# Optimization experiments

Hardware: AMD Instinct MI355X
Metric: run time of the kernel (lower is better)

Reference implementation:

```python
import jax, jax.numpy as jnp
import numpy as np

N = 50000   # nodes
E = 800000  # edges (avg degree 16)
D = 256     # node feature dim
H = 4       # heads per layer
C = 64      # per-head channels
L = 3       # depth
SCALE = 1.0 / (C ** 0.5)


def setup_inputs() -> dict:
    key = jax.random.key(0)
    ks = jax.random.split(key, 11)
    w = 0.05
    return {
        "x": jax.random.normal(ks[0], (N, D), jnp.float32),
        "edge_index": jax.random.randint(ks[1], (2, E), 0, N, dtype=jnp.int32),
        "Wq": jax.random.normal(ks[2], (L, D, H * C), jnp.float32) * w,
        "bq": jax.random.normal(ks[3], (L, H * C), jnp.float32) * w,
        "Wk": jax.random.normal(ks[4], (L, D, H * C), jnp.float32) * w,
        "bk": jax.random.normal(ks[5], (L, H * C), jnp.float32) * w,
        "Wv": jax.random.normal(ks[6], (L, D, H * C), jnp.float32) * w,
        "bv": jax.random.normal(ks[7], (L, H * C), jnp.float32) * w,
        "Ws": jax.random.normal(ks[8], (L, D, H * C), jnp.float32) * w,
        "bs": jax.random.normal(ks[9], (L, H * C), jnp.float32) * w,
    }


def _segment_softmax(alpha, seg, num_segments):
    # alpha: [E, H], seg: [E] destination node ids
    amax = jax.ops.segment_max(alpha, seg, num_segments=num_segments)  # [N, H]
    amax = jnp.where(jnp.isfinite(amax), amax, 0.0)  # isolated nodes -> -inf
    ex = jnp.exp(alpha - amax[seg])
    denom = jax.ops.segment_sum(ex, seg, num_segments=num_segments)  # [N, H]
    return ex / (denom[seg] + 1e-16)


def reference(x, edge_index, Wq, bq, Wk, bk, Wv, bv, Ws, bs):
    # PyG TransformerConv, heads=H, concat=True, root_weight=True, no edge features.
    src = edge_index[0]  # message source j
    dst = edge_index[1]  # message target i
    h = x
    for l in range(L):
        q = (h @ Wq[l] + bq[l]).reshape(N, H, C)
        k = (h @ Wk[l] + bk[l]).reshape(N, H, C)
        v = (h @ Wv[l] + bv[l]).reshape(N, H, C)
        # per-edge attention logits [E, H]
        alpha = jnp.einsum('ehc,ehc->eh', q[dst], k[src]) * SCALE
        attn = _segment_softmax(alpha, dst, N)
        # weighted message aggregation: [E, H, C] -> [N, H, C]
        msg = v[src] * attn[..., None]
        agg = jax.ops.segment_sum(msg, dst, num_segments=N).reshape(N, H * C)
        h = jax.nn.relu(agg + h @ Ws[l] + bs[l])
    return h
```

## Files before the change

### kernel.cpp

```cpp
#include <hip/hip_runtime.h>
#include <hip/hip_bf16.h>
#include <math.h>

#define N_NODES 50000
#define N_EDGES 800000
#define ATT_SCALE 0.125f

typedef __attribute__((ext_vector_type(8))) short bf16x8;
typedef __attribute__((ext_vector_type(4))) float f32x4;

__device__ __forceinline__ unsigned short f2bf(float f) {
  __hip_bfloat16 h = __float2bfloat16(f);
  unsigned short u; __builtin_memcpy(&u, &h, 2); return u;
}
__device__ __forceinline__ float bf2f(unsigned short u) {
  __hip_bfloat16 h; __builtin_memcpy(&h, &u, 2); return __bfloat162float(h);
}
__device__ __forceinline__ void gload16(const void* g, void* l) {
  __builtin_amdgcn_global_load_lds(
      (const __attribute__((address_space(1))) unsigned int*)g,
      (__attribute__((address_space(3))) unsigned int*)l, 16, 0, 0);
}

__global__ void zero_int(int* __restrict__ p, int n) {
  int i = blockIdx.x * blockDim.x + threadIdx.x;
  if (i < n) p[i] = 0;
}

__global__ void hist_kernel(const int* __restrict__ dst, int* __restrict__ counts, int e) {
  int i = blockIdx.x * blockDim.x + threadIdx.x;
  if (i < e) atomicAdd(&counts[dst[i]], 1);
}

__global__ __launch_bounds__(1024) void scan1_kernel(const int* __restrict__ counts,
                                                     int* __restrict__ offsets,
                                                     int* __restrict__ btot, int n) {
  __shared__ int wsum[16];
  const int tid = threadIdx.x;
  const int lane = tid & 63, wid = tid >> 6;
  int idx = blockIdx.x * 1024 + tid;
  int v = (idx < n) ? counts[idx] : 0;
  int s = v;
#pragma unroll
  for (int off = 1; off < 64; off <<= 1) {
    int t = __shfl_up(s, off);
    if (lane >= off) s += t;
  }
  if (lane == 63) wsum[wid] = s;
  __syncthreads();
  if (wid == 0) {
    int wsv = (lane < 16) ? wsum[lane] : 0;
#pragma unroll
    for (int off = 1; off < 16; off <<= 1) {
      int t = __shfl_up(wsv, off);
      if (lane >= off) wsv += t;
    }
    if (lane < 16) wsum[lane] = wsv;
  }
  __syncthreads();
  int wbase = (wid > 0) ? wsum[wid - 1] : 0;
  if (idx < n) offsets[idx] = wbase + s - v;
  if (tid == 0) btot[blockIdx.x] = wsum[15];
}

__global__ __launch_bounds__(64) void scan2_kernel(int* __restrict__ btot, int nb) {
  int lane = threadIdx.x;
  int v = (lane < nb) ? btot[lane] : 0;
  int s = v;
#pragma unroll
  for (int off = 1; off < 64; off <<= 1) {
    int t = __shfl_up(s, off);
    if (lane >= off) s += t;
  }
  if (lane < nb) btot[lane] = s - v;
}

__global__ void scan3_kernel(int* __restrict__ offsets, int* __restrict__ cursor,
                             const int* __restrict__ btot, int n) {
  int i = blockIdx.x * blockDim.x + threadIdx.x;
  if (i < n) {
    int o = offsets[i] + btot[i >> 10];
    offsets[i] = o;
    cursor[i] = o;
  }
}

__global__ __launch_bounds__(1024) void scan_kernel(const int* __restrict__ counts,
                                                    int* __restrict__ offsets,
                                                    int* __restrict__ cursor, int n) {
  __shared__ int wsum[16];
  const int tid = threadIdx.x;
  const int lane = tid & 63, wid = tid >> 6;
  int carry = 0;
  for (int base = 0; base < n; base += 1024) {
    int idx = base + tid;
    int v = (idx < n) ? counts[idx] : 0;
    int s = v;
#pragma unroll
    for (int off = 1; off < 64; off <<= 1) {
      int t = __shfl_up(s, off);
      if (lane >= off) s += t;
    }
    if (lane == 63) wsum[wid] = s;
    __syncthreads();
    if (wid == 0) {
      int wsv = (lane < 16) ? wsum[lane] : 0;
#pragma unroll
      for (int off = 1; off < 16; off <<= 1) {
        int t = __shfl_up(wsv, off);
        if (lane >= off) wsv += t;
      }
      if (lane < 16) wsum[lane] = wsv;
    }
    __syncthreads();
    int wbase = (wid > 0) ? wsum[wid - 1] : 0;
    if (idx < n) {
      int ex = carry + wbase + s - v;
      offsets[idx] = ex;
      cursor[idx] = ex;
    }
    int total = wsum[15];
    __syncthreads();
    carry += total;
  }
  if (tid == 0) offsets[n] = carry;
}

__global__ void fill_kernel(const int* __restrict__ src, const int* __restrict__ dst,
                            int* __restrict__ cursor, int* __restrict__ ssrc, int e) {
  int i = blockIdx.x * blockDim.x + threadIdx.x;
  if (i < e) {
    int d = dst[i];
    int slot = atomicAdd(&cursor[d], 1);
    ssrc[slot] = src[i];
  }
}

__global__ void convert_x_kernel(const float* __restrict__ x,
                                 unsigned short* __restrict__ Ahi,
                                 unsigned short* __restrict__ Alo) {
  int t = blockIdx.x * blockDim.x + threadIdx.x;
  int row = t >> 6, g = (t & 63) * 4;
  if (row >= N_NODES) return;
  float4 xv = *(const float4*)(x + (size_t)row * 256 + g);
  ushort4 hi, lo;
  hi.x = f2bf(xv.x); lo.x = f2bf(xv.x - bf2f(hi.x));
  hi.y = f2bf(xv.y); lo.y = f2bf(xv.y - bf2f(hi.y));
  hi.z = f2bf(xv.z); lo.z = f2bf(xv.z - bf2f(hi.z));
  hi.w = f2bf(xv.w); lo.w = f2bf(xv.w - bf2f(hi.w));
  *(ushort4*)(Ahi + (size_t)row * 256 + g) = hi;
  *(ushort4*)(Alo + (size_t)row * 256 + g) = lo;
}

__global__ void convert_w_kernel(const float* __restrict__ Wq, const float* __restrict__ Wk,
                                 const float* __restrict__ Wv, const float* __restrict__ Ws,
                                 unsigned short* __restrict__ Bexp) {
  int t = blockIdx.x * blockDim.x + threadIdx.x;
  if (t >= 3 * 256 * 1024) return;
  int n = t & 1023;
  int k = (t >> 10) & 255;
  int l = t >> 18;
  const float* W = (n < 256) ? Wq : (n < 512) ? Wk : (n < 768) ? Wv : Ws;
  float w = W[l * 65536 + k * 256 + (n & 255)];
  unsigned short hi = f2bf(w);
  unsigned short lo = f2bf(w - bf2f(hi));
  unsigned short* row = Bexp + ((size_t)l * 1024 + n) * 768;
  row[k] = hi; row[256 + k] = lo; row[512 + k] = hi;
}

__global__ __launch_bounds__(256) void bgemm_kernel(
    const unsigned short* __restrict__ Ahi,
    const unsigned short* __restrict__ Alo,
    const unsigned short* __restrict__ B,
    const float* __restrict__ bq, const float* __restrict__ bk,
    const float* __restrict__ bv, const float* __restrict__ bs,
    int layer,
    unsigned short* __restrict__ Qb,
    unsigned short* __restrict__ Kb,
    unsigned short* __restrict__ Vb,
    float* __restrict__ Sf) {
  __shared__ __align__(16) char lds[49152];
  char* Al  = lds;
  char* Bl1 = lds + 16384;
  char* Bl2 = lds + 32768;

  const int orig = blockIdx.x;
  const int swz = (orig & 7) * 391 + (orig >> 3);
  const int nb = swz & 7;
  const int m0 = (swz >> 3) * 128;

  const int tid = threadIdx.x;
  const int wid = tid >> 6;
  const int lane = tid & 63;
  const int l15 = lane & 15, lhi = lane >> 4;
  const int wr = wid >> 1, wc = wid & 1;

  const char* Ag_hi = (const char*)Ahi;
  const char* Ag_lo = (const char*)Alo;
  const char* Bg = (const char*)(B + ((size_t)layer * 1024 + nb * 128) * 768);

  f32x4 acc[4][4];
#pragma unroll
  for (int m = 0; m < 4; m++)
#pragma unroll
    for (int n = 0; n < 4; n++) acc[m][n] = (f32x4){0.f, 0.f, 0.f, 0.f};

  const int swzl = (l15 & 7) << 4;

  for (int kt4 = 0; kt4 < 4; kt4++) {
    const int ka2 = kt4 * 128;
#pragma unroll
    for (int i = 0; i < 4; i++) {
      int o = tid * 16 + i * 4096;
      int row = o >> 7;
      int sg = ((o >> 4) & 7) ^ (row & 7);
      gload16(Ag_hi + (size_t)(m0 + row) * 512 + ka2 + sg * 16, Al  + wid * 1024 + i * 4096);
      gload16(Bg + (size_t)row * 1536 + ka2 + sg * 16,          Bl1 + wid * 1024 + i * 4096);
      gload16(Bg + (size_t)row * 1536 + 512 + ka2 + sg * 16,    Bl2 + wid * 1024 + i * 4096);
    }
    __syncthreads();

    bf16x8 af[2][4], bfrag[2][4];
#pragma unroll
    for (int kk = 0; kk < 2; kk++)
#pragma unroll
      for (int m = 0; m < 4; m++) {
        af[kk][m]    = *(const bf16x8*)(Al  + (wr * 64 + m * 16 + l15) * 128 + ((kk * 64 + lhi * 16) ^ swzl));
        bfrag[kk][m] = *(const bf16x8*)(Bl1 + (wc * 64 + m * 16 + l15) * 128 + ((kk * 64 + lhi * 16) ^ swzl));
      }
#pragma unroll
    for (int kk = 0; kk < 2; kk++)
#pragma unroll
      for (int m = 0; m < 4; m++)
#pragma unroll
        for (int n = 0; n < 4; n++)
          acc[m][n] = __builtin_amdgcn_mfma_f32_16x16x32_bf16(af[kk][m], bfrag[kk][n], acc[m][n], 0, 0, 0);
#pragma unroll
    for (int kk = 0; kk < 2; kk++)
#pragma unroll
      for (int m = 0; m < 4; m++)
        bfrag[kk][m] = *(const bf16x8*)(Bl2 + (wc * 64 + m * 16 + l15) * 128 + ((kk * 64 + lhi * 16) ^ swzl));
#pragma unroll
    for (int kk = 0; kk < 2; kk++)
#pragma unroll
      for (int m = 0; m < 4; m++)
#pragma unroll
        for (int n = 0; n < 4; n++)
          acc[m][n] = __builtin_amdgcn_mfma_f32_16x16x32_bf16(af[kk][m], bfrag[kk][n], acc[m][n], 0, 0, 0);
    __syncthreads();
  }

  for (int kt4 = 0; kt4 < 4; kt4++) {
    const int ka2 = kt4 * 128;
#pragma unroll
    for (int i = 0; i < 4; i++) {
      int o = tid * 16 + i * 4096;
      int row = o >> 7;
      int sg = ((o >> 4) & 7) ^ (row & 7);
      gload16(Ag_lo + (size_t)(m0 + row) * 512 + ka2 + sg * 16, Al  + wid * 1024 + i * 4096);
      gload16(Bg + (size_t)row * 1536 + 1024 + ka2 + sg * 16,   Bl1 + wid * 1024 + i * 4096);
    }
    __syncthreads();

    bf16x8 af[2][4], bfrag[2][4];
#pragma unroll
    for (int kk = 0; kk < 2; kk++)
#pragma unroll
      for (int m = 0; m < 4; m++) {
        af[kk][m]    = *(const bf16x8*)(Al  + (wr * 64 + m * 16 + l15) * 128 + ((kk * 64 + lhi * 16) ^ swzl));
        bfrag[kk][m] = *(const bf16x8*)(Bl1 + (wc * 64 + m * 16 + l15) * 128 + ((kk * 64 + lhi * 16) ^ swzl));
      }
#pragma unroll
    for (int kk = 0; kk < 2; kk++)
#pragma unroll
      for (int m = 0; m < 4; m++)
#pragma unroll
        for (int n = 0; n < 4; n++)
          acc[m][n] = __builtin_amdgcn_mfma_f32_16x16x32_bf16(af[kk][m], bfrag[kk][n], acc[m][n], 0, 0, 0);
    __syncthreads();
  }

  const float* bias = ((nb < 2) ? bq : (nb < 4) ? bk : (nb < 6) ? bv : bs) + layer * 256 + (nb & 1) * 128;
  float bn[4];
#pragma unroll
  for (int n = 0; n < 4; n++) bn[n] = bias[wc * 64 + n * 16 + l15];

  const int col = (nb & 1) * 128 + wc * 64 + l15;
  if (nb < 6) {
    unsigned short* T = (nb < 2) ? Qb : (nb < 4) ? Kb : Vb;
#pragma unroll
    for (int m = 0; m < 4; m++) {
#pragma unroll
      for (int r = 0; r < 4; r++) {
        int row = m0 + wr * 64 + m * 16 + lhi * 4 + r;
        if (row < N_NODES) {
          unsigned short* orow = T + (size_t)row * 256 + col;
#pragma unroll
          for (int n = 0; n < 4; n++) orow[n * 16] = f2bf(acc[m][n][r] + bn[n]);
        }
      }
    }
  } else {
#pragma unroll
    for (int m = 0; m < 4; m++) {
#pragma unroll
      for (int r = 0; r < 4; r++) {
        int row = m0 + wr * 64 + m * 16 + lhi * 4 + r;
        if (row < N_NODES) {
          float* orow = Sf + (size_t)row * 256 + col;
#pragma unroll
          for (int n = 0; n < 4; n++) orow[n * 16] = acc[m][n][r] + bn[n];
        }
      }
    }
  }
}

template <int MODE>
__global__ __launch_bounds__(256) void attn_kernel(
    const unsigned short* __restrict__ Qb,
    const unsigned short* __restrict__ Kb,
    const unsigned short* __restrict__ Vb,
    const float* __restrict__ Sf,
    const int* __restrict__ offsets,
    const int* __restrict__ counts,
    const int* __restrict__ ssrc,
    float* __restrict__ hout,
    unsigned short* __restrict__ Ahi,
    unsigned short* __restrict__ Alo) {
  int wv = threadIdx.x >> 6;
  int lane = threadIdx.x & 63;
  int i = blockIdx.x * 4 + wv;
  if (i >= N_NODES) return;

  const int off = (lane >> 4) * 64 + (lane & 15) * 4;

  ushort4 qb = *(const ushort4*)(Qb + (size_t)i * 256 + off);
  float4 q = make_float4(bf2f(qb.x), bf2f(qb.y), bf2f(qb.z), bf2f(qb.w));

  float mC[4] = {-1e30f, -1e30f, -1e30f, -1e30f};
  float sC[4] = {0.f, 0.f, 0.f, 0.f};
  float4 aC[4];
#pragma unroll
  for (int u = 0; u < 4; u++) aC[u] = make_float4(0.f, 0.f, 0.f, 0.f);

  const int beg = offsets[i];
  const int cnt = counts[i];
  int e = 0;
  for (; e + 4 <= cnt; e += 4) {
    int j[4];
#pragma unroll
    for (int u = 0; u < 4; u++) j[u] = ssrc[beg + e + u];
    ushort4 kk[4], vv[4];
#pragma unroll
    for (int u = 0; u < 4; u++) {
      kk[u] = *(const ushort4*)(Kb + (size_t)j[u] * 256 + off);
      vv[u] = *(const ushort4*)(Vb + (size_t)j[u] * 256 + off);
    }
    float p[4];
#pragma unroll
    for (int u = 0; u < 4; u++)
      p[u] = q.x * bf2f(kk[u].x) + q.y * bf2f(kk[u].y) +
             q.z * bf2f(kk[u].z) + q.w * bf2f(kk[u].w);
#pragma unroll
    for (int u = 0; u < 4; u++) p[u] += __shfl_xor(p[u], 1);
#pragma unroll
    for (int u = 0; u < 4; u++) p[u] += __shfl_xor(p[u], 2);
#pragma unroll
    for (int u = 0; u < 4; u++) p[u] += __shfl_xor(p[u], 4);
#pragma unroll
    for (int u = 0; u < 4; u++) p[u] += __shfl_xor(p[u], 8);
#pragma unroll
    for (int u = 0; u < 4; u++) {
      float pv = p[u] * ATT_SCALE;
      float mn = fmaxf(mC[u], pv);
      float c = __expf(mC[u] - mn);
      float w = __expf(pv - mn);
      sC[u] = sC[u] * c + w;
      aC[u].x = aC[u].x * c + w * bf2f(vv[u].x);
      aC[u].y = aC[u].y * c + w * bf2f(vv[u].y);
      aC[u].z = aC[u].z * c + w * bf2f(vv[u].z);
      aC[u].w = aC[u].w * c + w * bf2f(vv[u].w);
      mC[u] = mn;
    }
  }
  for (; e < cnt; e++) {
    int j1 = ssrc[beg + e];
    ushort4 k1 = *(const ushort4*)(Kb + (size_t)j1 * 256 + off);
    ushort4 v1 = *(const ushort4*)(Vb + (size_t)j1 * 256 + off);
    float p1 = q.x * bf2f(k1.x) + q.y * bf2f(k1.y) + q.z * bf2f(k1.z) + q.w * bf2f(k1.w);
    p1 += __shfl_xor(p1, 1);
    p1 += __shfl_xor(p1, 2);
    p1 += __shfl_xor(p1, 4);
    p1 += __shfl_xor(p1, 8);
    p1 *= ATT_SCALE;
    float mn = fmaxf(mC[0], p1); float c = __expf(mC[0] - mn); float w = __expf(p1 - mn);
    sC[0] = sC[0] * c + w;
    aC[0].x = aC[0].x * c + w * bf2f(v1.x);
    aC[0].y = aC[0].y * c + w * bf2f(v1.y);
    aC[0].z = aC[0].z * c + w * bf2f(v1.z);
    aC[0].w = aC[0].w * c + w * bf2f(v1.w);
    mC[0] = mn;
  }

  float mm = fmaxf(fmaxf(mC[0], mC[1]), fmaxf(mC[2], mC[3]));
  float s = 0.f;
  float4 a = make_float4(0.f, 0.f, 0.f, 0.f);
#pragma unroll
  for (int u = 0; u < 4; u++) {
    float c = __expf(mC[u] - mm);
    s += sC[u] * c;
    a.x += aC[u].x * c;
    a.y += aC[u].y * c;
    a.z += aC[u].z * c;
    a.w += aC[u].w * c;
  }

  float4 sk = *(const float4*)(Sf + (size_t)i * 256 + off);
  float inv = 1.f / (s + 1e-16f);
  float4 o = make_float4(fmaxf(a.x * inv + sk.x, 0.f),
                         fmaxf(a.y * inv + sk.y, 0.f),
                         fmaxf(a.z * inv + sk.z, 0.f),
                         fmaxf(a.w * inv + sk.w, 0.f));
  if (MODE == 0) {
    *(float4*)(hout + (size_t)i * 256 + off) = o;
  } else {
    ushort4 hi, lo;
    hi.x = f2bf(o.x); lo.x = f2bf(o.x - bf2f(hi.x));
    hi.y = f2bf(o.y); lo.y = f2bf(o.y - bf2f(hi.y));
    hi.z = f2bf(o.z); lo.z = f2bf(o.z - bf2f(hi.z));
    hi.w = f2bf(o.w); lo.w = f2bf(o.w - bf2f(hi.w));
    *(ushort4*)(Ahi + (size_t)i * 256 + off) = hi;
    *(ushort4*)(Alo + (size_t)i * 256 + off) = lo;
  }
}

#define BM 128
#define BN 128
#define BK 16
__global__ __launch_bounds__(256) void gemm_kernel(
    const float* __restrict__ X,
    const float* __restrict__ Wq, const float* __restrict__ Wk,
    const float* __restrict__ Wv, const float* __restrict__ Ws,
    const float* __restrict__ bq, const float* __restrict__ bk,
    const float* __restrict__ bv, const float* __restrict__ bs,
    int layer, float* __restrict__ out) {
  __shared__ __align__(16) float As[BK][BM + 4];
  __shared__ __align__(16) float Bs[BK][BN + 4];
  const int m0 = blockIdx.x * BM;
  const int n0 = blockIdx.y * BN;
  const int wsel = n0 >> 8;
  const float* W;
  const float* bias;
  if (wsel == 0)      { W = Wq; bias = bq; }
  else if (wsel == 1) { W = Wk; bias = bk; }
  else if (wsel == 2) { W = Wv; bias = bv; }
  else                { W = Ws; bias = bs; }
  W += (size_t)layer * 256 * 256;
  bias += (size_t)layer * 256;
  const int nc0 = n0 & 255;
  const int tid = threadIdx.x;
  const int tx = tid & 15;
  const int ty = tid >> 4;
  float acc[8][8];
#pragma unroll
  for (int i = 0; i < 8; i++)
#pragma unroll
    for (int j = 0; j < 8; j++) acc[i][j] = 0.f;
  for (int k0 = 0; k0 < 256; k0 += BK) {
#pragma unroll
    for (int i = 0; i < 8; i++) {
      int idx = tid + i * 256;
      int r = idx >> 4, c = idx & 15;
      int gr = m0 + r;
      As[c][r] = (gr < N_NODES) ? X[(size_t)gr * 256 + k0 + c] : 0.f;
    }
#pragma unroll
    for (int i = 0; i < 8; i++) {
      int idx = tid + i * 256;
      int r = idx >> 7, c = idx & 127;
      Bs[r][c] = W[(size_t)(k0 + r) * 256 + nc0 + c];
    }
    __syncthreads();
#pragma unroll
    for (int k = 0; k < BK; k++) {
      float4 a0 = *(const float4*)&As[k][ty * 8];
      float4 a1 = *(const float4*)&As[k][ty * 8 + 4];
      float4 b0 = *(const float4*)&Bs[k][tx * 8];
      float4 b1 = *(const float4*)&Bs[k][tx * 8 + 4];
      float a[8] = {a0.x, a0.y, a0.z, a0.w, a1.x, a1.y, a1.z, a1.w};
      float b[8] = {b0.x, b0.y, b0.z, b0.w, b1.x, b1.y, b1.z, b1.w};
#pragma unroll
      for (int mi = 0; mi < 8; mi++)
#pragma unroll
        for (int ni = 0; ni < 8; ni++) acc[mi][ni] = fmaf(a[mi], b[ni], acc[mi][ni]);
    }
    __syncthreads();
  }
  float bl[8];
#pragma unroll
  for (int ni = 0; ni < 8; ni++) bl[ni] = bias[nc0 + tx * 8 + ni];
#pragma unroll
  for (int mi = 0; mi < 8; mi++) {
    int row = m0 + ty * 8 + mi;
    if (row < N_NODES) {
      float* orow = out + (size_t)row * 1024 + n0 + tx * 8;
      float4 o0 = make_float4(acc[mi][0] + bl[0], acc[mi][1] + bl[1],
                              acc[mi][2] + bl[2], acc[mi][3] + bl[3]);
      float4 o1 = make_float4(acc[mi][4] + bl[4], acc[mi][5] + bl[5],
                              acc[mi][6] + bl[6], acc[mi][7] + bl[7]);
      *(float4*)orow = o0;
      *(float4*)(orow + 4) = o1;
    }
  }
}

__global__ __launch_bounds__(256) void attn_legacy(
    const float* __restrict__ qkvs,
    const int* __restrict__ offsets,
    const int* __restrict__ counts,
    const int* __restrict__ ssrc,
    float* __restrict__ hout) {
  int wv = threadIdx.x >> 6;
  int lane = threadIdx.x & 63;
  int i = blockIdx.x * 4 + wv;
  if (i >= N_NODES) return;
  const int off = (lane >> 4) * 64 + (lane & 15) * 4;
  const float* base_i = qkvs + (size_t)i * 1024;
  float4 q = *(const float4*)(base_i + off);
  float m = -INFINITY, s = 0.f;
  float4 a = make_float4(0.f, 0.f, 0.f, 0.f);
  int beg = offsets[i];
  int cnt = counts[i];
  for (int e = 0; e < cnt; e++) {
    int j = ssrc[beg + e];
    const float* base_j = qkvs + (size_t)j * 1024;
    float4 k = *(const float4*)(base_j + 256 + off);
    float p = q.x * k.x + q.y * k.y + q.z * k.z + q.w * k.w;
    p += __shfl_xor(p, 1);
    p += __shfl_xor(p, 2);
    p += __shfl_xor(p, 4);
    p += __shfl_xor(p, 8);
    p *= ATT_SCALE;
    float4 v = *(const float4*)(base_j + 512 + off);
    float mn = fmaxf(m, p);
    float c = __expf(m - mn);
    float w = __expf(p - mn);
    s = s * c + w;
    a.x = a.x * c + w * v.x;
    a.y = a.y * c + w * v.y;
    a.z = a.z * c + w * v.z;
    a.w = a.w * c + w * v.w;
    m = mn;
  }
  float4 sk = *(const float4*)(base_i + 768 + off);
  float inv = 1.f / (s + 1e-16f);
  float4 o = make_float4(fmaxf(a.x * inv + sk.x, 0.f),
                         fmaxf(a.y * inv + sk.y, 0.f),
                         fmaxf(a.z * inv + sk.z, 0.f),
                         fmaxf(a.w * inv + sk.w, 0.f));
  *(float4*)(hout + (size_t)i * 256 + off) = o;
}

extern "C" void kernel_launch(void* const* d_in, const int* in_sizes, int n_in,
                              void* d_out, int out_size, void* d_ws, size_t ws_size,
                              hipStream_t stream) {
  (void)in_sizes; (void)n_in; (void)out_size;
  const float* x   = (const float*)d_in[0];
  const int*   ei  = (const int*)d_in[1];
  const float* Wq  = (const float*)d_in[2];
  const float* bq  = (const float*)d_in[3];
  const float* Wk  = (const float*)d_in[4];
  const float* bk  = (const float*)d_in[5];
  const float* Wv  = (const float*)d_in[6];
  const float* bv  = (const float*)d_in[7];
  const float* Ws_ = (const float*)d_in[8];
  const float* bs  = (const float*)d_in[9];
  float* out = (float*)d_out;

  const int* src = ei;
  const int* dst = ei + N_EDGES;
  char* ws = (char*)d_ws;

  const size_t NEED = 187768064ull;
  bool big = ws_size >= NEED;

  if (big) {
    unsigned short* Qb   = (unsigned short*)(ws + 0);
    unsigned short* Kb   = (unsigned short*)(ws + 25600000);
    unsigned short* Vb   = (unsigned short*)(ws + 51200000);
    float*          Sf   = (float*)(ws + 76800000);
    unsigned short* Ahi  = (unsigned short*)(ws + 128000000);
    unsigned short* Alo  = (unsigned short*)(ws + 153624576);
    unsigned short* Bexp = (unsigned short*)(ws + 179249152);
    int* counts = (int*)(ws + 183967744);
    int* offs   = (int*)(ws + 184167744);
    int* cursor = (int*)(ws + 184367808);
    int* ssrc   = (int*)(ws + 184567808);
    int* btot   = (int*)(ws + 187767808);

    zero_int<<<(N_NODES + 255) / 256, 256, 0, stream>>>(counts, N_NODES);
    hist_kernel<<<(N_EDGES + 255) / 256, 256, 0, stream>>>(dst, counts, N_EDGES);
    scan1_kernel<<<(N_NODES + 1023) / 1024, 1024, 0, stream>>>(counts, offs, btot, N_NODES);
    scan2_kernel<<<1, 64, 0, stream>>>(btot, (N_NODES + 1023) / 1024);
    scan3_kernel<<<(N_NODES + 255) / 256, 256, 0, stream>>>(offs, cursor, btot, N_NODES);
    fill_kernel<<<(N_EDGES + 255) / 256, 256, 0, stream>>>(src, dst, cursor, ssrc, N_EDGES);

    convert_w_kernel<<<3072, 256, 0, stream>>>(Wq, Wk, Wv, Ws_, Bexp);
    convert_x_kernel<<<(N_NODES * 64 + 255) / 256, 256, 0, stream>>>(x, Ahi, Alo);

    for (int l = 0; l < 3; l++) {
      bgemm_kernel<<<3128, 256, 0, stream>>>(Ahi, Alo, Bexp, bq, bk, bv, bs, l, Qb, Kb, Vb, Sf);
      if (l < 2)
        attn_kernel<1><<<(N_NODES + 3) / 4, 256, 0, stream>>>(Qb, Kb, Vb, Sf, offs, counts, ssrc,
                                                              nullptr, Ahi, Alo);
      else
        attn_kernel<0><<<(N_NODES + 3) / 4, 256, 0, stream>>>(Qb, Kb, Vb, Sf, offs, counts, ssrc,
                                                              out, nullptr, nullptr);
    }
  } else {
    float* qkvs   = (float*)(ws + 0);
    float* hbuf   = (float*)(ws + 204800000);
    int*   counts = (int*)(ws + 256000000);
    int*   offs   = (int*)(ws + 256200064);
    int*   cursor = (int*)(ws + 256400128);
    int*   ssrc   = (int*)(ws + 256600192);

    zero_int<<<(N_NODES + 255) / 256, 256, 0, stream>>>(counts, N_NODES);
    hist_kernel<<<(N_EDGES + 255) / 256, 256, 0, stream>>>(dst, counts, N_EDGES);
    scan_kernel<<<1, 1024, 0, stream>>>(counts, offs, cursor, N_NODES);
    fill_kernel<<<(N_EDGES + 255) / 256, 256, 0, stream>>>(src, dst, cursor, ssrc, N_EDGES);

    dim3 ggrid((N_NODES + BM - 1) / BM, 1024 / BN);
    for (int l = 0; l < 3; l++) {
      const float* hin = (l == 0) ? x : hbuf;
      float* hout = (l == 2) ? out : hbuf;
      gemm_kernel<<<ggrid, 256, 0, stream>>>(hin, Wq, Wk, Wv, Ws_, bq, bk, bv, bs, l, qkvs);
      attn_legacy<<<(N_NODES + 3) / 4, 256, 0, stream>>>(qkvs, offs, counts, ssrc, hout);
    }
  }
}
```

Measured before the change: 812.0 us.

## Interleave K and V rows and sort per-node neighbor lists by source

K and V projections are now stored interleaved in a single [N,512] bf16 buffer, so each gathered neighbor's key and value sit in adjacent memory and share DRAM pages and TLB entries. A new per-node insertion sort orders the CSR neighbor lists by source id, which makes the gather addresses more monotonic and deterministic across runs. The sort adds a serial per-thread kernel whose cost is small at an average degree of 16. Gather locality across different destination nodes is unchanged, since the sources are random.

```diff
diff --git a/kernel.cpp b/kernel.cpp
--- a/kernel.cpp
+++ b/kernel.cpp
@@ -133,6 +133,22 @@
     int d = dst[i];
     int slot = atomicAdd(&cursor[d], 1);
     ssrc[slot] = src[i];
+  }
+}
+
+__global__ void sort_kernel(const int* __restrict__ offsets, const int* __restrict__ counts,
+                            int* __restrict__ ssrc) {
+  int i = blockIdx.x * blockDim.x + threadIdx.x;
+  if (i >= N_NODES) return;
+  int beg = offsets[i], cnt = counts[i];
+  for (int a = 1; a < cnt; a++) {
+    int key = ssrc[beg + a];
+    int b = a - 1;
+    while (b >= 0 && ssrc[beg + b] > key) {
+      ssrc[beg + b + 1] = ssrc[beg + b];
+      b--;
+    }
+    ssrc[beg + b + 1] = key;
   }
 }
 
@@ -176,8 +192,7 @@
     const float* __restrict__ bv, const float* __restrict__ bs,
     int layer,
     unsigned short* __restrict__ Qb,
-    unsigned short* __restrict__ Kb,
-    unsigned short* __restrict__ Vb,
+    unsigned short* __restrict__ KVb,
     float* __restrict__ Sf) {
   __shared__ __align__(16) char lds[49152];
   char* Al  = lds;
@@ -286,15 +301,28 @@
   for (int n = 0; n < 4; n++) bn[n] = bias[wc * 64 + n * 16 + l15];
 
   const int col = (nb & 1) * 128 + wc * 64 + l15;
-  if (nb < 6) {
-    unsigned short* T = (nb < 2) ? Qb : (nb < 4) ? Kb : Vb;
+  if (nb < 2) {
 #pragma unroll
     for (int m = 0; m < 4; m++) {
 #pragma unroll
       for (int r = 0; r < 4; r++) {
         int row = m0 + wr * 64 + m * 16 + lhi * 4 + r;
         if (row < N_NODES) {
-          unsigned short* orow = T + (size_t)row * 256 + col;
+          unsigned short* orow = Qb + (size_t)row * 256 + col;
+#pragma unroll
+          for (int n = 0; n < 4; n++) orow[n * 16] = f2bf(acc[m][n][r] + bn[n]);
+        }
+      }
+    }
+  } else if (nb < 6) {
+    const int col512 = ((nb >= 4) ? 256 : 0) + col;
+#pragma unroll
+    for (int m = 0; m < 4; m++) {
+#pragma unroll
+      for (int r = 0; r < 4; r++) {
+        int row = m0 + wr * 64 + m * 16 + lhi * 4 + r;
+        if (row < N_NODES) {
+          unsigned short* orow = KVb + (size_t)row * 512 + col512;
 #pragma unroll
           for (int n = 0; n < 4; n++) orow[n * 16] = f2bf(acc[m][n][r] + bn[n]);
         }
@@ -319,8 +347,7 @@
 template <int MODE>
 __global__ __launch_bounds__(256) void attn_kernel(
     const unsigned short* __restrict__ Qb,
-    const unsigned short* __restrict__ Kb,
-    const unsigned short* __restrict__ Vb,
+    const unsigned short* __restrict__ KVb,
     const float* __restrict__ Sf,
     const int* __restrict__ offsets,
     const int* __restrict__ counts,
@@ -354,8 +381,9 @@
     ushort4 kk[4], vv[4];
 #pragma unroll
     for (int u = 0; u < 4; u++) {
-      kk[u] = *(const ushort4*)(Kb + (size_t)j[u] * 256 + off);
-      vv[u] = *(const ushort4*)(Vb + (size_t)j[u] * 256 + off);
+      const unsigned short* base = KVb + (size_t)j[u] * 512;
+      kk[u] = *(const ushort4*)(base + off);
+      vv[u] = *(const ushort4*)(base + 256 + off);
     }
     float p[4];
 #pragma unroll
@@ -386,8 +414,9 @@
   }
   for (; e < cnt; e++) {
     int j1 = ssrc[beg + e];
-    ushort4 k1 = *(const ushort4*)(Kb + (size_t)j1 * 256 + off);
-    ushort4 v1 = *(const ushort4*)(Vb + (size_t)j1 * 256 + off);
+    const unsigned short* base = KVb + (size_t)j1 * 512;
+    ushort4 k1 = *(const ushort4*)(base + off);
+    ushort4 v1 = *(const ushort4*)(base + 256 + off);
     float p1 = q.x * bf2f(k1.x) + q.y * bf2f(k1.y) + q.z * bf2f(k1.z) + q.w * bf2f(k1.w);
     p1 += __shfl_xor(p1, 1);
     p1 += __shfl_xor(p1, 2);
@@ -587,8 +616,7 @@
 
   if (big) {
     unsigned short* Qb   = (unsigned short*)(ws + 0);
-    unsigned short* Kb   = (unsigned short*)(ws + 25600000);
-    unsigned short* Vb   = (unsigned short*)(ws + 51200000);
+    unsigned short* KVb  = (unsigned short*)(ws + 25600000);
     float*          Sf   = (float*)(ws + 76800000);
     unsigned short* Ahi  = (unsigned short*)(ws + 128000000);
     unsigned short* Alo  = (unsigned short*)(ws + 153624576);
@@ -605,17 +633,18 @@
     scan2_kernel<<<1, 64, 0, stream>>>(btot, (N_NODES + 1023) / 1024);
     scan3_kernel<<<(N_NODES + 255) / 256, 256, 0, stream>>>(offs, cursor, btot, N_NODES);
     fill_kernel<<<(N_EDGES + 255) / 256, 256, 0, stream>>>(src, dst, cursor, ssrc, N_EDGES);
+    sort_kernel<<<(N_NODES + 255) / 256, 256, 0, stream>>>(offs, counts, ssrc);
 
     convert_w_kernel<<<3072, 256, 0, stream>>>(Wq, Wk, Wv, Ws_, Bexp);
     convert_x_kernel<<<(N_NODES * 64 + 255) / 256, 256, 0, stream>>>(x, Ahi, Alo);
 
     for (int l = 0; l < 3; l++) {
-      bgemm_kernel<<<3128, 256, 0, stream>>>(Ahi, Alo, Bexp, bq, bk, bv, bs, l, Qb, Kb, Vb, Sf);
+      bgemm_kernel<<<3128, 256, 0, stream>>>(Ahi, Alo, Bexp, bq, bk, bv, bs, l, Qb, KVb, Sf);
       if (l < 2)
-        attn_kernel<1><<<(N_NODES + 3) / 4, 256, 0, stream>>>(Qb, Kb, Vb, Sf, offs, counts, ssrc,
+        attn_kernel<1><<<(N_NODES + 3) / 4, 256, 0, stream>>>(Qb, KVb, Sf, offs, counts, ssrc,
                                                               nullptr, Ahi, Alo);
       else
-        attn_kernel<0><<<(N_NODES + 3) / 4, 256, 0, stream>>>(Qb, Kb, Vb, Sf, offs, counts, ssrc,
+        attn_kernel<0><<<(N_NODES + 3) / 4, 256, 0, stream>>>(Qb, KVb, Sf, offs, counts, ssrc,
                                                               out, nullptr, nullptr);
     }
   } else {
```

Result: slower. 896.9 us (+10.5%).
